# Performance work log

Hardware: AMD Instinct MI355X
Metric: run time of the kernel (lower is better)

The kernel has to match this reference:

```python
import jax, jax.numpy as jnp
import numpy as np

N, L = 32, 2048
C_S, C_E, C_H, K, NRES = 384, 32, 128, 7, 20
C_IN = C_S + C_E  # 416
EPS = 1e-8


def setup_inputs() -> dict:
    key = jax.random.key(0)
    ks = jax.random.split(key, 32)
    s = 0.02
    d = {}
    d['aa_seq'] = jax.random.randint(ks[0], (L,), 0, NRES)
    d['sfea_tns'] = jax.random.normal(ks[1], (N, L, C_S), jnp.float32)
    d['sfea_tns_init'] = jax.random.normal(ks[2], (N, L, C_S), jnp.float32)
    d['encd_tns'] = jax.random.normal(ks[3], (N, L, C_E), jnp.float32)
    d['quat_tns'] = jax.random.normal(ks[4], (N, L, 4), jnp.float32)
    d['trsl_tns'] = jax.random.normal(ks[5], (N, L, 3), jnp.float32)
    # FrameHead linears
    d['Wq'] = jax.random.normal(ks[6], (C_IN, 4), jnp.float32) * s
    d['bq'] = jnp.zeros((4,), jnp.float32)
    d['Wt'] = jax.random.normal(ks[7], (C_IN, 3), jnp.float32) * s
    d['bt'] = jnp.zeros((3,), jnp.float32)
    # 20 per-residue-type AngleHead experts, stacked on leading axis
    d['Wa1'] = jax.random.normal(ks[8], (NRES, C_IN, C_H), jnp.float32) * s
    d['ba1'] = jnp.zeros((NRES, C_H), jnp.float32)
    d['Wa2'] = jax.random.normal(ks[9], (NRES, C_IN, C_H), jnp.float32) * s
    d['ba2'] = jnp.zeros((NRES, C_H), jnp.float32)
    d['Wb1a'] = jax.random.normal(ks[10], (NRES, C_H, C_H), jnp.float32) * s
    d['bb1a'] = jnp.zeros((NRES, C_H), jnp.float32)
    d['Wb1b'] = jax.random.normal(ks[11], (NRES, C_H, C_H), jnp.float32) * s
    d['bb1b'] = jnp.zeros((NRES, C_H), jnp.float32)
    d['Wb2a'] = jax.random.normal(ks[12], (NRES, C_H, C_H), jnp.float32) * s
    d['bb2a'] = jnp.zeros((NRES, C_H), jnp.float32)
    d['Wb2b'] = jax.random.normal(ks[13], (NRES, C_H, C_H), jnp.float32) * s
    d['bb2b'] = jnp.zeros((NRES, C_H), jnp.float32)
    d['Wout'] = jax.random.normal(ks[14], (NRES, C_H, K * 2), jnp.float32) * s
    d['bout'] = jnp.zeros((NRES, K * 2), jnp.float32)
    return d


def _qnorm(q):
    return q * jax.lax.rsqrt(jnp.sum(q * q, -1, keepdims=True) + EPS)


def _quat_mul(q, p):
    w1, x1, y1, z1 = jnp.split(q, 4, -1)
    w2, x2, y2, z2 = jnp.split(p, 4, -1)
    return jnp.concatenate([
        w1 * w2 - x1 * x2 - y1 * y2 - z1 * z2,
        w1 * x2 + x1 * w2 + y1 * z2 - z1 * y2,
        w1 * y2 - x1 * z2 + y1 * w2 + z1 * x2,
        w1 * z2 + x1 * y2 - y1 * x2 + z1 * w2], -1)


def _quat_rotate(q, v):
    # rotate vector v by unit quaternion q = (w, xyz)
    w, qv = q[..., :1], q[..., 1:]
    t = 2.0 * jnp.cross(qv, v)
    return v + w * t + jnp.cross(qv, t)


def _angle_net(sfcd, sfcd_init, aa, Wa1, ba1, Wa2, ba2,
               Wb1a, bb1a, Wb1b, bb1b, Wb2a, bb2a, Wb2b, bb2b, Wout, bout):
    # residue-type routed AngleHead: gather each token's expert weights by aa index
    g = lambda W: jnp.take(W, aa, axis=0)  # [L, ...]
    relu = jax.nn.relu
    a = (jnp.einsum('nlc,lch->nlh', relu(sfcd), g(Wa1)) + g(ba1)
         + jnp.einsum('nlc,lch->nlh', relu(sfcd_init), g(Wa2)) + g(ba2))
    # residual block 1
    h = jnp.einsum('nlh,lhk->nlk', relu(a), g(Wb1a)) + g(bb1a)
    a = a + jnp.einsum('nlh,lhk->nlk', relu(h), g(Wb1b)) + g(bb1b)
    # residual block 2
    h = jnp.einsum('nlh,lhk->nlk', relu(a), g(Wb2a)) + g(bb2a)
    a = a + jnp.einsum('nlh,lhk->nlk', relu(h), g(Wb2b)) + g(bb2b)
    out = jnp.einsum('nlh,lhk->nlk', relu(a), g(Wout)) + g(bout)  # [N,L,2K]
    ang = out.reshape(out.shape[0], out.shape[1], K, 2)
    norm = jnp.sqrt(jnp.sum(ang * ang, -1, keepdims=True) + 1e-12)
    return ang / norm


def reference(aa_seq, sfea_tns, sfea_tns_init, encd_tns, quat_tns, trsl_tns,
              Wq, bq, Wt, bt, Wa1, ba1, Wa2, ba2, Wb1a, bb1a, Wb1b, bb1b,
              Wb2a, bb2a, Wb2b, bb2b, Wout, bout):
    sfcd = jnp.concatenate([sfea_tns, encd_tns], -1)          # [N,L,C_IN]
    sfcd_init = jnp.concatenate([sfea_tns_init, encd_tns], -1)
    # FrameHead: quaternion/translation update signals
    quat_upd = sfcd @ Wq + bq                                  # [N,L,4]
    trsl_upd = sfcd @ Wt + bt                                  # [N,L,3]
    q_old = _qnorm(quat_tns)
    quat_new = _qnorm(_quat_mul(q_old, _qnorm(quat_upd)))
    trsl_new = trsl_tns + _quat_rotate(q_old, trsl_upd)
    angl_tns = _angle_net(sfcd, sfcd_init, aa_seq, Wa1, ba1, Wa2, ba2,
                          Wb1a, bb1a, Wb1b, bb1b, Wb2a, bb2a, Wb2b, bb2b,
                          Wout, bout)
    return quat_new, trsl_new, angl_tns, quat_upd
```

## Files before the change

### kernel.cpp

```cpp
#include <hip/hip_runtime.h>

#define L_SEQ 2048
#define CS 384
#define CE 32
#define CIN 416
#define CH 128
#define NRES 20

#define ABST 136
#define PADN 2068
#define NB2  1034

#define PERM_REGION 4608
#define WA_PER (CH*CIN)
#define WB_PER (CH*CH)
#define WO_PER (16*CH)
#define OFF_WA1T 0
#define OFF_WA2T (NRES*WA_PER)
#define OFF_WB1AT (2*NRES*WA_PER)
#define OFF_WB1BT (OFF_WB1AT + 1*NRES*WB_PER)
#define OFF_WB2AT (OFF_WB1AT + 2*NRES*WB_PER)
#define OFF_WB2BT (OFF_WB1AT + 3*NRES*WB_PER)
#define OFF_WOUTT (OFF_WB1AT + 4*NRES*WB_PER)
#define TOTW (OFF_WOUTT + NRES*WO_PER)

#define OUT_TR 262144
#define OUT_ANG 458752
#define OUT_QU 1376256

#define LOSCALE 4096.0f
#define ILOSCALE (1.0f/4096.0f)
#define F16MIN 6.1035156e-5f

typedef _Float16 f16x8 __attribute__((ext_vector_type(8)));
typedef _Float16 f16x4 __attribute__((ext_vector_type(4)));
typedef float f32x4 __attribute__((ext_vector_type(4)));

#define MFMA16 __builtin_amdgcn_mfma_f32_16x16x32_f16

static __device__ __forceinline__ void split1(float x, _Float16& h, _Float16& l) {
  _Float16 hi = (__builtin_fabsf(x) < F16MIN) ? (_Float16)0.f : (_Float16)x;
  h = hi;
  l = (_Float16)((x - (float)hi) * LOSCALE);
}

__global__ __launch_bounds__(256) void quat_head(
    const float* __restrict__ sfea, const float* __restrict__ encd,
    const float* __restrict__ quat, const float* __restrict__ trsl,
    const float* __restrict__ Wq, const float* __restrict__ bq,
    const float* __restrict__ Wt, const float* __restrict__ bt,
    float* __restrict__ out) {
  const int wv   = threadIdx.x >> 6;
  const int lane = threadIdx.x & 63;
  const size_t idx = (size_t)blockIdx.x * 4 + wv;
  const float* __restrict__ srow = sfea + idx * CS;

  float q0=0,q1=0,q2=0,q3=0,t0=0,t1=0,t2=0;
  #pragma unroll
  for (int cc = 0; cc < 6; ++cc) {
    const int ch = cc*64 + lane;
    const float s = srow[ch];
    const float4 wq = *reinterpret_cast<const float4*>(Wq + (size_t)ch*4);
    const float* wt = Wt + (size_t)ch*3;
    q0 += s*wq.x; q1 += s*wq.y; q2 += s*wq.z; q3 += s*wq.w;
    t0 += s*wt[0]; t1 += s*wt[1]; t2 += s*wt[2];
  }
  if (lane < CE) {
    const float s = encd[idx*CE + lane];
    const int ch = CS + lane;
    const float4 wq = *reinterpret_cast<const float4*>(Wq + (size_t)ch*4);
    const float* wt = Wt + (size_t)ch*3;
    q0 += s*wq.x; q1 += s*wq.y; q2 += s*wq.z; q3 += s*wq.w;
    t0 += s*wt[0]; t1 += s*wt[1]; t2 += s*wt[2];
  }
  #pragma unroll
  for (int off = 1; off < 64; off <<= 1) {
    q0 += __shfl_xor(q0, off); q1 += __shfl_xor(q1, off);
    q2 += __shfl_xor(q2, off); q3 += __shfl_xor(q3, off);
    t0 += __shfl_xor(t0, off); t1 += __shfl_xor(t1, off);
    t2 += __shfl_xor(t2, off);
  }
  if (lane == 0) {
    const float u0 = q0 + bq[0], u1 = q1 + bq[1], u2 = q2 + bq[2], u3 = q3 + bq[3];
    const float v0 = t0 + bt[0], v1 = t1 + bt[1], v2 = t2 + bt[2];
    float a0 = quat[idx*4+0], a1 = quat[idx*4+1], a2 = quat[idx*4+2], a3 = quat[idx*4+3];
    const float rq = rsqrtf(a0*a0+a1*a1+a2*a2+a3*a3 + 1e-8f);
    a0*=rq; a1*=rq; a2*=rq; a3*=rq;
    const float ru = rsqrtf(u0*u0+u1*u1+u2*u2+u3*u3 + 1e-8f);
    const float p0=u0*ru, p1=u1*ru, p2=u2*ru, p3=u3*ru;
    const float mw = a0*p0 - a1*p1 - a2*p2 - a3*p3;
    const float mx = a0*p1 + a1*p0 + a2*p3 - a3*p2;
    const float my = a0*p2 - a1*p3 + a2*p0 + a3*p1;
    const float mz = a0*p3 + a1*p2 - a2*p1 + a3*p0;
    const float rm = rsqrtf(mw*mw+mx*mx+my*my+mz*mz + 1e-8f);
    out[idx*4+0]=mw*rm; out[idx*4+1]=mx*rm; out[idx*4+2]=my*rm; out[idx*4+3]=mz*rm;
    const float tx = 2.f*(a2*v2 - a3*v1);
    const float ty = 2.f*(a3*v0 - a1*v2);
    const float tz = 2.f*(a1*v1 - a2*v0);
    out[OUT_TR + idx*3+0] = trsl[idx*3+0] + v0 + a0*tx + (a2*tz - a3*ty);
    out[OUT_TR + idx*3+1] = trsl[idx*3+1] + v1 + a0*ty + (a3*tx - a1*tz);
    out[OUT_TR + idx*3+2] = trsl[idx*3+2] + v2 + a0*tz + (a1*ty - a2*tx);
    out[OUT_QU + idx*4+0]=u0; out[OUT_QU + idx*4+1]=u1;
    out[OUT_QU + idx*4+2]=u2; out[OUT_QU + idx*4+3]=u3;
  }
}

__global__ __launch_bounds__(1024) void build_perm(const int* __restrict__ aa_seq,
                                                   unsigned short* __restrict__ perm) {
  __shared__ int cnt[NRES*32];
  __shared__ int woff[NRES*32];
  __shared__ int poff_s[NRES];
  __shared__ int ctot_s[NRES];
  const int t = threadIdx.x;
  const int wv = t >> 6, lane = t & 63;

  for (int i = t; i < PADN; i += 1024) perm[i] = 0;

  int aav[2];
  #pragma unroll
  for (int h = 0; h < 2; ++h) {
    const int W = wv + h*16;
    aav[h] = aa_seq[W*64 + lane];
    #pragma unroll
    for (int a = 0; a < NRES; ++a) {
      const unsigned long long m = __ballot(aav[h] == a);
      if (lane == a) cnt[a*32 + W] = (int)__popcll(m);
    }
  }
  __syncthreads();
  if (t < 32) {
    int tot = 0;
    if (t < NRES) {
      #pragma unroll
      for (int W = 0; W < 32; ++W) tot += cnt[t*32 + W];
    }
    const int pa = (t < NRES) ? ((tot + 1) & ~1) : 0;
    int s = pa;
    #pragma unroll
    for (int o = 1; o < 32; o <<= 1) {
      const int u = __shfl_up(s, o);
      if (lane >= o) s += u;
    }
    if (t < NRES) { poff_s[t] = s - pa; ctot_s[t] = tot; }
    for (int a = 0; a < NRES; ++a) {
      const int v0 = cnt[a*32 + t];
      int v = v0;
      #pragma unroll
      for (int o = 1; o < 32; o <<= 1) {
        const int u = __shfl_up(v, o);
        if (lane >= o) v += u;
      }
      woff[a*32 + t] = poff_s[a] + v - v0;
    }
  }
  __syncthreads();
  const unsigned long long ltmask = (lane == 0) ? 0ull : (~0ull >> (64 - lane));
  #pragma unroll
  for (int h = 0; h < 2; ++h) {
    const int W = wv + h*16;
    const int a = aav[h];
    int pos = 0;
    #pragma unroll
    for (int aq = 0; aq < NRES; ++aq) {
      const unsigned long long m = __ballot(a == aq);
      if (a == aq) pos = woff[aq*32 + W] + (int)__popcll(m & ltmask);
    }
    const unsigned short lv = (unsigned short)(W*64 + lane);
    perm[pos] = lv;
    if ((ctot_s[a] & 1) && pos == poff_s[a] + ctot_s[a] - 1) perm[pos + 1] = lv;
  }
}

__global__ __launch_bounds__(256) void convert_w(
    const float* __restrict__ Wa1, const float* __restrict__ Wa2,
    const float* __restrict__ Wb1a, const float* __restrict__ Wb1b,
    const float* __restrict__ Wb2a, const float* __restrict__ Wb2b,
    const float* __restrict__ Wout, _Float16* __restrict__ wsw) {
  const int idx = blockIdx.x * 256 + threadIdx.x;
  if (idx >= TOTW) return;
  float v;
  if (idx < OFF_WB1AT) {
    const int which = (idx < OFF_WA2T) ? 0 : 1;
    const float* W = which ? Wa2 : Wa1;
    int r = idx - which * OFF_WA2T;
    const int aa = r / WA_PER; r -= aa * WA_PER;
    const int h = r / CIN;     const int c = r - h * CIN;
    v = W[((size_t)aa*CIN + c)*CH + h];
  } else if (idx < OFF_WOUTT) {
    int q = idx - OFF_WB1AT;
    const int which = q / (NRES*WB_PER);
    int r = q - which * (NRES*WB_PER);
    const float* W = (which==0)?Wb1a:(which==1)?Wb1b:(which==2)?Wb2a:Wb2b;
    const int aa = r / WB_PER; r -= aa * WB_PER;
    const int h = r / CH;      const int c = r - h * CH;
    v = W[((size_t)aa*CH + c)*CH + h];
  } else {
    int r = idx - OFF_WOUTT;
    const int aa = r / WO_PER; r -= aa * WO_PER;
    const int kk = r / CH;     const int c = r - kk * CH;
    v = (kk < 14) ? Wout[((size_t)aa*CH + c)*14 + kk] : 0.f;
  }
  _Float16 h, l; split1(v, h, l);
  wsw[idx] = h;
  wsw[(size_t)TOTW + idx] = l;
}

static __device__ __forceinline__ void fold(f32x4 acc[2][2], const f32x4 accL[2][2],
                                            float b0, float b1) {
  #pragma unroll
  for (int m = 0; m < 2; ++m)
    #pragma unroll
    for (int i = 0; i < 4; ++i) {
      acc[m][0][i] += accL[m][0][i]*ILOSCALE + b0;
      acc[m][1][i] += accL[m][1][i]*ILOSCALE + b1;
    }
}

static __device__ __forceinline__ void store_relu_pair(_Float16* dh, _Float16* dl,
    const f32x4 acc[2][2], int lane, int h0) {
  const int lr = lane & 15;
  const int r0 = (lane >> 4) << 2;
  #pragma unroll
  for (int m = 0; m < 2; ++m)
    #pragma unroll
    for (int p = 0; p < 2; ++p)
      #pragma unroll
      for (int i = 0; i < 4; ++i) {
        const float v = fmaxf(acc[m][p][i], 0.f);
        _Float16 hh, ll; split1(v, hh, ll);
        const int idx = (m*16 + r0 + i)*ABST + h0 + p*16 + lr;
        dh[idx] = hh; dl[idx] = ll;
      }
}

template<int S>
static __device__ __forceinline__ void gemm_dual(
    const _Float16* aH0, const _Float16* aL0,
    const _Float16* aH1, const _Float16* aL1,
    const _Float16* __restrict__ wH,
    int kbase, int nks,
    f32x4 acc0[2][2], f32x4 acc0L[2][2],
    f32x4 acc1[2][2], f32x4 acc1L[2][2],
    int lane, int h0) {
  const int lr = lane & 15;
  const int lk = (lane >> 4) << 3;
  #pragma unroll
  for (int ks = 0; ks < nks; ++ks) {
    const int kl = ks*32 + lk;
    const int kg = kbase + kl;
    const _Float16* p0 = wH + (size_t)(h0+lr)*S + kg;
    const _Float16* p1 = wH + (size_t)(h0+16+lr)*S + kg;
    const f16x8 b0h = *(const f16x8*)p0;
    const f16x8 b0l = *(const f16x8*)(p0 + TOTW);
    const f16x8 b1h = *(const f16x8*)p1;
    const f16x8 b1l = *(const f16x8*)(p1 + TOTW);
#define DOPOS(AH, AL, AC, ACL) { \
    const f16x8 a0h = *(const f16x8*)(AH + lr*ABST + kl); \
    const f16x8 a0l = *(const f16x8*)(AL + lr*ABST + kl); \
    const f16x8 a1h = *(const f16x8*)(AH + (lr+16)*ABST + kl); \
    const f16x8 a1l = *(const f16x8*)(AL + (lr+16)*ABST + kl); \
    AC[0][0]  = MFMA16(a0h, b0h, AC[0][0], 0,0,0); \
    ACL[0][0] = MFMA16(a0h, b0l, ACL[0][0], 0,0,0); \
    ACL[0][0] = MFMA16(a0l, b0h, ACL[0][0], 0,0,0); \
    AC[1][0]  = MFMA16(a1h, b0h, AC[1][0], 0,0,0); \
    ACL[1][0] = MFMA16(a1h, b0l, ACL[1][0], 0,0,0); \
    ACL[1][0] = MFMA16(a1l, b0h, ACL[1][0], 0,0,0); \
    AC[0][1]  = MFMA16(a0h, b1h, AC[0][1], 0,0,0); \
    ACL[0][1] = MFMA16(a0h, b1l, ACL[0][1], 0,0,0); \
    ACL[0][1] = MFMA16(a0l, b1h, ACL[0][1], 0,0,0); \
    AC[1][1]  = MFMA16(a1h, b1h, AC[1][1], 0,0,0); \
    ACL[1][1] = MFMA16(a1h, b1l, ACL[1][1], 0,0,0); \
    ACL[1][1] = MFMA16(a1l, b1h, ACL[1][1], 0,0,0); }
    DOPOS(aH0, aL0, acc0, acc0L)
    DOPOS(aH1, aL1, acc1, acc1L)
#undef DOPOS
  }
}

static __device__ __forceinline__ void stage_row128(
    const float* __restrict__ row, _Float16* dH, _Float16* dL, int n, int sj) {
  #pragma unroll
  for (int q2 = 0; q2 < 2; ++q2) {
    const int cl = q2*64 + sj*8;
    const float4 v0 = *(const float4*)(row + cl);
    const float4 v1 = *(const float4*)(row + cl + 4);
    const float xs[8] = {v0.x,v0.y,v0.z,v0.w,v1.x,v1.y,v1.z,v1.w};
    f16x8 h8, l8;
    #pragma unroll
    for (int e = 0; e < 8; ++e) {
      _Float16 hh, ll; split1(fmaxf(xs[e], 0.f), hh, ll);
      h8[e] = hh; l8[e] = ll;
    }
    *(f16x8*)(dH + n*ABST + cl) = h8;
    *(f16x8*)(dL + n*ABST + cl) = l8;
  }
}

static __device__ __forceinline__ void stage_encd(
    const float* __restrict__ erow,
    _Float16* sH, _Float16* sL, _Float16* iH, _Float16* iL, int n, int sj) {
  const int cl = sj*4;
  const float4 v = *(const float4*)(erow + cl);
  const float xs[4] = {v.x, v.y, v.z, v.w};
  f16x4 h4, l4;
  #pragma unroll
  for (int e = 0; e < 4; ++e) {
    _Float16 hh, ll; split1(fmaxf(xs[e], 0.f), hh, ll);
    h4[e] = hh; l4[e] = ll;
  }
  *(f16x4*)(sH + n*ABST + cl) = h4;  *(f16x4*)(sL + n*ABST + cl) = l4;
  *(f16x4*)(iH + n*ABST + cl) = h4;  *(f16x4*)(iL + n*ABST + cl) = l4;
}

__global__ __launch_bounds__(256, 2) void fah_main(
    const int* __restrict__ aa_seq, const unsigned short* __restrict__ perm,
    const float* __restrict__ sfea, const float* __restrict__ sfei,
    const float* __restrict__ encd,
    const float* __restrict__ ba1, const float* __restrict__ ba2,
    const float* __restrict__ bb1a, const float* __restrict__ bb1b,
    const float* __restrict__ bb2a, const float* __restrict__ bb2b,
    const float* __restrict__ bout,
    const _Float16* __restrict__ wsw,
    float* __restrict__ out) {
  __shared__ __align__(16) _Float16 sf0H[32*ABST], sf0L[32*ABST];
  __shared__ __align__(16) _Float16 in0H[32*ABST], in0L[32*ABST];
  __shared__ __align__(16) _Float16 sf1H[32*ABST], sf1L[32*ABST];
  __shared__ __align__(16) _Float16 in1H[32*ABST], in1L[32*ABST];
  _Float16 *ab0H = sf0H, *ab0L = sf0L, *hb0H = in0H, *hb0L = in0L;
  _Float16 *ab1H = sf1H, *ab1L = sf1L, *hb1H = in1H, *hb1L = in1L;

  const int orig = blockIdx.x;
  const int xcd = orig & 7, i8 = orig >> 3;
  const int sp = (xcd < 2 ? xcd*130 : 260 + (xcd-2)*129) + i8;
  const int l0 = perm[2*sp], l1 = perm[2*sp+1];
  const int aa = aa_seq[l0];

  const int t = threadIdx.x;
  const int lane = t & 63, wv = t >> 6;
  const int lr = lane & 15, lk = (lane >> 4) << 3, h0 = wv * 32;
  const int n = t >> 3, sj = t & 7;

  const f32x4 zz = {0.f, 0.f, 0.f, 0.f};
  f32x4 accA0[2][2], accA0L[2][2], accA1[2][2], accA1L[2][2];
  #pragma unroll
  for (int m = 0; m < 2; ++m) {
    accA0[m][0]=zz; accA0[m][1]=zz; accA0L[m][0]=zz; accA0L[m][1]=zz;
    accA1[m][0]=zz; accA1[m][1]=zz; accA1L[m][0]=zz; accA1L[m][1]=zz;
  }

  const _Float16* wsA1 = wsw + OFF_WA1T + (size_t)aa*WA_PER;
  const _Float16* wsA2 = wsw + OFF_WA2T + (size_t)aa*WA_PER;

  #pragma unroll
  for (int ck = 0; ck < 4; ++ck) {
    const int koff = ck * 128;
    if (ck < 3) {
      stage_row128(sfea + ((size_t)n*L_SEQ + l0)*CS + koff, sf0H, sf0L, n, sj);
      stage_row128(sfei + ((size_t)n*L_SEQ + l0)*CS + koff, in0H, in0L, n, sj);
      stage_row128(sfea + ((size_t)n*L_SEQ + l1)*CS + koff, sf1H, sf1L, n, sj);
      stage_row128(sfei + ((size_t)n*L_SEQ + l1)*CS + koff, in1H, in1L, n, sj);
    } else {
      stage_encd(encd + ((size_t)n*L_SEQ + l0)*CE, sf0H, sf0L, in0H, in0L, n, sj);
      stage_encd(encd + ((size_t)n*L_SEQ + l1)*CE, sf1H, sf1L, in1H, in1L, n, sj);
    }
    __syncthreads();
    const int nks = (ck < 3) ? 4 : 1;
    gemm_dual<CIN>(sf0H, sf0L, sf1H, sf1L, wsA1, koff, nks,
                   accA0, accA0L, accA1, accA1L, lane, h0);
    gemm_dual<CIN>(in0H, in0L, in1H, in1L, wsA2, koff, nks,
                   accA0, accA0L, accA1, accA1L, lane, h0);
    __syncthreads();
  }

  {
    const float b0v = ba1[aa*CH + h0 + lr]      + ba2[aa*CH + h0 + lr];
    const float b1v = ba1[aa*CH + h0 + 16 + lr] + ba2[aa*CH + h0 + 16 + lr];
    fold(accA0, accA0L, b0v, b1v);
    fold(accA1, accA1L, b0v, b1v);
    store_relu_pair(ab0H, ab0L, accA0, lane, h0);
    store_relu_pair(ab1H, ab1L, accA1, lane, h0);
  }
  __syncthreads();

  {
    f32x4 c0[2][2], c0L[2][2], c1[2][2], c1L[2][2];
    #pragma unroll
    for (int m = 0; m < 2; ++m) { c0[m][0]=zz;c0[m][1]=zz;c0L[m][0]=zz;c0L[m][1]=zz;
                                  c1[m][0]=zz;c1[m][1]=zz;c1L[m][0]=zz;c1L[m][1]=zz; }
    gemm_dual<CH>(ab0H, ab0L, ab1H, ab1L, wsw + OFF_WB1AT + (size_t)aa*WB_PER, 0, 4,
                  c0, c0L, c1, c1L, lane, h0);
    const float B0 = bb1a[aa*CH + h0 + lr], B1 = bb1a[aa*CH + h0 + 16 + lr];
    fold(c0, c0L, B0, B1); fold(c1, c1L, B0, B1);
    store_relu_pair(hb0H, hb0L, c0, lane, h0);
    store_relu_pair(hb1H, hb1L, c1, lane, h0);
  }
  __syncthreads();
  {
    f32x4 c0L[2][2], c1L[2][2];
    #pragma unroll
    for (int m = 0; m < 2; ++m) { c0L[m][0]=zz;c0L[m][1]=zz;c1L[m][0]=zz;c1L[m][1]=zz; }
    gemm_dual<CH>(hb0H, hb0L, hb1H, hb1L, wsw + OFF_WB1BT + (size_t)aa*WB_PER, 0, 4,
                  accA0, c0L, accA1, c1L, lane, h0);
    const float B0 = bb1b[aa*CH + h0 + lr], B1 = bb1b[aa*CH + h0 + 16 + lr];
    fold(accA0, c0L, B0, B1); fold(accA1, c1L, B0, B1);
    store_relu_pair(ab0H, ab0L, accA0, lane, h0);
    store_relu_pair(ab1H, ab1L, accA1, lane, h0);
  }
  __syncthreads();
  {
    f32x4 c0[2][2], c0L[2][2], c1[2][2], c1L[2][2];
    #pragma unroll
    for (int m = 0; m < 2; ++m) { c0[m][0]=zz;c0[m][1]=zz;c0L[m][0]=zz;c0L[m][1]=zz;
                                  c1[m][0]=zz;c1[m][1]=zz;c1L[m][0]=zz;c1L[m][1]=zz; }
    gemm_dual<CH>(ab0H, ab0L, ab1H, ab1L, wsw + OFF_WB2AT + (size_t)aa*WB_PER, 0, 4,
                  c0, c0L, c1, c1L, lane, h0);
    const float B0 = bb2a[aa*CH + h0 + lr], B1 = bb2a[aa*CH + h0 + 16 + lr];
    fold(c0, c0L, B0, B1); fold(c1, c1L, B0, B1);
    store_relu_pair(hb0H, hb0L, c0, lane, h0);
    store_relu_pair(hb1H, hb1L, c1, lane, h0);
  }
  __syncthreads();
  {
    f32x4 c0L[2][2], c1L[2][2];
    #pragma unroll
    for (int m = 0; m < 2; ++m) { c0L[m][0]=zz;c0L[m][1]=zz;c1L[m][0]=zz;c1L[m][1]=zz; }
    gemm_dual<CH>(hb0H, hb0L, hb1H, hb1L, wsw + OFF_WB2BT + (size_t)aa*WB_PER, 0, 4,
                  accA0, c0L, accA1, c1L, lane, h0);
    const float B0 = bb2b[aa*CH + h0 + lr], B1 = bb2b[aa*CH + h0 + 16 + lr];
    fold(accA0, c0L, B0, B1); fold(accA1, c1L, B0, B1);
    store_relu_pair(ab0H, ab0L, accA0, lane, h0);
    store_relu_pair(ab1H, ab1L, accA1, lane, h0);
  }
  __syncthreads();

  {
    const int pos  = wv >> 1;
    const int half = wv & 1;
    const _Float16* aH = pos ? ab1H : ab0H;
    const _Float16* aL = pos ? ab1L : ab0L;
    const int lsel = pos ? l1 : l0;
    f32x4 o = zz, oL = zz;
    #pragma unroll
    for (int ks = 0; ks < 4; ++ks) {
      const int k = ks*32 + lk;
      const f16x8 ah = *(const f16x8*)(aH + (half*16 + lr)*ABST + k);
      const f16x8 al = *(const f16x8*)(aL + (half*16 + lr)*ABST + k);
      const _Float16* p = wsw + OFF_WOUTT + (size_t)aa*WO_PER + (size_t)lr*CH + k;
      const f16x8 bh = *(const f16x8*)p;
      const f16x8 bl = *(const f16x8*)(p + TOTW);
      o  = MFMA16(ah, bh, o,  0,0,0);
      oL = MFMA16(ah, bl, oL, 0,0,0);
      oL = MFMA16(al, bh, oL, 0,0,0);
    }
    const float bo = (lr < 14) ? bout[aa*14 + lr] : 0.f;
    #pragma unroll
    for (int i = 0; i < 4; ++i) {
      const float v  = o[i] + oL[i]*ILOSCALE + bo;
      const float pv = __shfl_xor(v, 1);
      const float r  = rsqrtf(v*v + pv*pv + 1e-12f);
      if (lr < 14) {
        const int nrow = half*16 + ((lane >> 4) << 2) + i;
        out[OUT_ANG + (size_t)nrow*(L_SEQ*14) + (size_t)lsel*14 + lr] = v*r;
      }
    }
  }
}

extern "C" void kernel_launch(void* const* d_in, const int* in_sizes, int n_in,
                              void* d_out, int out_size, void* d_ws, size_t ws_size,
                              hipStream_t stream) {
  const int*   aa   = (const int*)  d_in[0];
  const float* sfea = (const float*)d_in[1];
  const float* sfei = (const float*)d_in[2];
  const float* encd = (const float*)d_in[3];
  const float* quat = (const float*)d_in[4];
  const float* trsl = (const float*)d_in[5];
  const float* Wq   = (const float*)d_in[6];
  const float* bq   = (const float*)d_in[7];
  const float* Wt   = (const float*)d_in[8];
  const float* bt   = (const float*)d_in[9];
  const float* Wa1  = (const float*)d_in[10];
  const float* ba1  = (const float*)d_in[11];
  const float* Wa2  = (const float*)d_in[12];
  const float* ba2  = (const float*)d_in[13];
  const float* Wb1a = (const float*)d_in[14];
  const float* bb1a = (const float*)d_in[15];
  const float* Wb1b = (const float*)d_in[16];
  const float* bb1b = (const float*)d_in[17];
  const float* Wb2a = (const float*)d_in[18];
  const float* bb2a = (const float*)d_in[19];
  const float* Wb2b = (const float*)d_in[20];
  const float* bb2b = (const float*)d_in[21];
  const float* Wout = (const float*)d_in[22];
  const float* bout = (const float*)d_in[23];
  float* out = (float*)d_out;

  unsigned short* perm = (unsigned short*)d_ws;
  _Float16* wsw = (_Float16*)((char*)d_ws + PERM_REGION);

  hipLaunchKernelGGL(build_perm, dim3(1), dim3(1024), 0, stream, aa, perm);
  hipLaunchKernelGGL(convert_w, dim3((TOTW + 255)/256), dim3(256), 0, stream,
                     Wa1, Wa2, Wb1a, Wb1b, Wb2a, Wb2b, Wout, wsw);
  hipLaunchKernelGGL(quat_head, dim3(16384), dim3(256), 0, stream,
                     sfea, encd, quat, trsl, Wq, bq, Wt, bt, out);
  hipLaunchKernelGGL(fah_main, dim3(NB2), dim3(256), 0, stream,
                     aa, perm, sfea, sfei, encd,
                     ba1, ba2, bb1a, bb1b, bb2a, bb2b, bout, wsw, out);
}
```

Before: 209.2 us.

## Prefetch next input chunk into registers during GEMM and use lighter barriers

The first-layer loop is unrolled by hand so the global loads for the next 128-column chunk of sfea/sfei (and encd) are issued into registers before the current chunk's MFMA work. The loaded values are converted and written to LDS after the following barrier. All __syncthreads are replaced with a macro that waits only on lgkmcnt before s_barrier, so outstanding global loads are not drained at each barrier. This hides global memory latency behind compute, at the cost of many more live VGPRs (32 float4 registers) under launch_bounds(256,2).

```diff
diff --git a/kernel.cpp b/kernel.cpp
--- a/kernel.cpp
+++ b/kernel.cpp
@@ -37,6 +37,8 @@
 typedef float f32x4 __attribute__((ext_vector_type(4)));
 
 #define MFMA16 __builtin_amdgcn_mfma_f32_16x16x32_f16
+
+#define BAR() { asm volatile("s_waitcnt lgkmcnt(0)" ::: "memory"); __builtin_amdgcn_s_barrier(); }
 
 static __device__ __forceinline__ void split1(float x, _Float16& h, _Float16& l) {
   _Float16 hi = (__builtin_fabsf(x) < F16MIN) ? (_Float16)0.f : (_Float16)x;
@@ -277,30 +279,28 @@
   }
 }
 
-static __device__ __forceinline__ void stage_row128(
+static __device__ __forceinline__ void wr8(const float4 v0, const float4 v1,
+    _Float16* dH, _Float16* dL, int n, int cl) {
+  const float xs[8] = {v0.x,v0.y,v0.z,v0.w,v1.x,v1.y,v1.z,v1.w};
+  f16x8 h8, l8;
+  #pragma unroll
+  for (int e = 0; e < 8; ++e) {
+    _Float16 hh, ll; split1(fmaxf(xs[e], 0.f), hh, ll);
+    h8[e] = hh; l8[e] = ll;
+  }
+  *(f16x8*)(dH + n*ABST + cl) = h8;
+  *(f16x8*)(dL + n*ABST + cl) = l8;
+}
+
+static __device__ __forceinline__ void stage_row_inline(
     const float* __restrict__ row, _Float16* dH, _Float16* dL, int n, int sj) {
-  #pragma unroll
-  for (int q2 = 0; q2 < 2; ++q2) {
-    const int cl = q2*64 + sj*8;
-    const float4 v0 = *(const float4*)(row + cl);
-    const float4 v1 = *(const float4*)(row + cl + 4);
-    const float xs[8] = {v0.x,v0.y,v0.z,v0.w,v1.x,v1.y,v1.z,v1.w};
-    f16x8 h8, l8;
-    #pragma unroll
-    for (int e = 0; e < 8; ++e) {
-      _Float16 hh, ll; split1(fmaxf(xs[e], 0.f), hh, ll);
-      h8[e] = hh; l8[e] = ll;
-    }
-    *(f16x8*)(dH + n*ABST + cl) = h8;
-    *(f16x8*)(dL + n*ABST + cl) = l8;
-  }
-}
-
-static __device__ __forceinline__ void stage_encd(
-    const float* __restrict__ erow,
+  wr8(*(const float4*)(row + sj*8),      *(const float4*)(row + sj*8 + 4),      dH, dL, n, sj*8);
+  wr8(*(const float4*)(row + 64 + sj*8), *(const float4*)(row + 64 + sj*8 + 4), dH, dL, n, 64 + sj*8);
+}
+
+static __device__ __forceinline__ void stage_encd_reg(const float4 v,
     _Float16* sH, _Float16* sL, _Float16* iH, _Float16* iL, int n, int sj) {
   const int cl = sj*4;
-  const float4 v = *(const float4*)(erow + cl);
   const float xs[4] = {v.x, v.y, v.z, v.w};
   f16x4 h4, l4;
   #pragma unroll
@@ -311,6 +311,16 @@
   *(f16x4*)(sH + n*ABST + cl) = h4;  *(f16x4*)(sL + n*ABST + cl) = l4;
   *(f16x4*)(iH + n*ABST + cl) = h4;  *(f16x4*)(iL + n*ABST + cl) = l4;
 }
+
+#define PF_ROW(BASE, OFF, V0, V1, V2, V3)                         \
+  V0 = *(const float4*)((BASE) + (OFF) + sj*8);                   \
+  V1 = *(const float4*)((BASE) + (OFF) + sj*8 + 4);               \
+  V2 = *(const float4*)((BASE) + (OFF) + 64 + sj*8);              \
+  V3 = *(const float4*)((BASE) + (OFF) + 64 + sj*8 + 4);
+
+#define WR_ROW(V0, V1, V2, V3, DH, DL)                            \
+  wr8(V0, V1, DH, DL, n, sj*8);                                   \
+  wr8(V2, V3, DH, DL, n, 64 + sj*8);
 
 __global__ __launch_bounds__(256, 2) void fah_main(
     const int* __restrict__ aa_seq, const unsigned short* __restrict__ perm,
@@ -340,6 +350,14 @@
   const int lr = lane & 15, lk = (lane >> 4) << 3, h0 = wv * 32;
   const int n = t >> 3, sj = t & 7;
 
+  const float* sfeaL0 = sfea + ((size_t)n*L_SEQ + l0)*CS;
+  const float* sfeaL1 = sfea + ((size_t)n*L_SEQ + l1)*CS;
+  const float* sfeiL0 = sfei + ((size_t)n*L_SEQ + l0)*CS;
+  const float* sfeiL1 = sfei + ((size_t)n*L_SEQ + l1)*CS;
+
+  const _Float16* wsA1 = wsw + OFF_WA1T + (size_t)aa*WA_PER;
+  const _Float16* wsA2 = wsw + OFF_WA2T + (size_t)aa*WA_PER;
+
   const f32x4 zz = {0.f, 0.f, 0.f, 0.f};
   f32x4 accA0[2][2], accA0L[2][2], accA1[2][2], accA1L[2][2];
   #pragma unroll
@@ -348,30 +366,56 @@
     accA1[m][0]=zz; accA1[m][1]=zz; accA1L[m][0]=zz; accA1L[m][1]=zz;
   }
 
-  const _Float16* wsA1 = wsw + OFF_WA1T + (size_t)aa*WA_PER;
-  const _Float16* wsA2 = wsw + OFF_WA2T + (size_t)aa*WA_PER;
-
-  #pragma unroll
-  for (int ck = 0; ck < 4; ++ck) {
-    const int koff = ck * 128;
-    if (ck < 3) {
-      stage_row128(sfea + ((size_t)n*L_SEQ + l0)*CS + koff, sf0H, sf0L, n, sj);
-      stage_row128(sfei + ((size_t)n*L_SEQ + l0)*CS + koff, in0H, in0L, n, sj);
-      stage_row128(sfea + ((size_t)n*L_SEQ + l1)*CS + koff, sf1H, sf1L, n, sj);
-      stage_row128(sfei + ((size_t)n*L_SEQ + l1)*CS + koff, in1H, in1L, n, sj);
-    } else {
-      stage_encd(encd + ((size_t)n*L_SEQ + l0)*CE, sf0H, sf0L, in0H, in0L, n, sj);
-      stage_encd(encd + ((size_t)n*L_SEQ + l1)*CE, sf1H, sf1L, in1H, in1L, n, sj);
-    }
-    __syncthreads();
-    const int nks = (ck < 3) ? 4 : 1;
-    gemm_dual<CIN>(sf0H, sf0L, sf1H, sf1L, wsA1, koff, nks,
-                   accA0, accA0L, accA1, accA1L, lane, h0);
-    gemm_dual<CIN>(in0H, in0L, in1H, in1L, wsA2, koff, nks,
-                   accA0, accA0L, accA1, accA1L, lane, h0);
-    __syncthreads();
-  }
-
+  float4 A00,A01,A02,A03, A10,A11,A12,A13;
+  float4 I00,I01,I02,I03, I10,I11,I12,I13;
+
+  stage_row_inline(sfeaL0, sf0H, sf0L, n, sj);
+  stage_row_inline(sfeiL0, in0H, in0L, n, sj);
+  stage_row_inline(sfeaL1, sf1H, sf1L, n, sj);
+  stage_row_inline(sfeiL1, in1H, in1L, n, sj);
+  PF_ROW(sfeaL0, 128, A00,A01,A02,A03)
+  PF_ROW(sfeaL1, 128, A10,A11,A12,A13)
+  PF_ROW(sfeiL0, 128, I00,I01,I02,I03)
+  PF_ROW(sfeiL1, 128, I10,I11,I12,I13)
+  BAR();
+
+  gemm_dual<CIN>(sf0H,sf0L,sf1H,sf1L, wsA1, 0, 4, accA0,accA0L,accA1,accA1L, lane, h0);
+  gemm_dual<CIN>(in0H,in0L,in1H,in1L, wsA2, 0, 4, accA0,accA0L,accA1,accA1L, lane, h0);
+  BAR();
+
+  WR_ROW(A00,A01,A02,A03, sf0H,sf0L)
+  WR_ROW(A10,A11,A12,A13, sf1H,sf1L)
+  WR_ROW(I00,I01,I02,I03, in0H,in0L)
+  WR_ROW(I10,I11,I12,I13, in1H,in1L)
+  PF_ROW(sfeaL0, 256, A00,A01,A02,A03)
+  PF_ROW(sfeaL1, 256, A10,A11,A12,A13)
+  PF_ROW(sfeiL0, 256, I00,I01,I02,I03)
+  PF_ROW(sfeiL1, 256, I10,I11,I12,I13)
+  BAR();
+
+  gemm_dual<CIN>(sf0H,sf0L,sf1H,sf1L, wsA1, 128, 4, accA0,accA0L,accA1,accA1L, lane, h0);
+  gemm_dual<CIN>(in0H,in0L,in1H,in1L, wsA2, 128, 4, accA0,accA0L,accA1,accA1L, lane, h0);
+  BAR();
+
+  WR_ROW(A00,A01,A02,A03, sf0H,sf0L)
+  WR_ROW(A10,A11,A12,A13, sf1H,sf1L)
+  WR_ROW(I00,I01,I02,I03, in0H,in0L)
+  WR_ROW(I10,I11,I12,I13, in1H,in1L)
+  float4 E0, E1;
+  E0 = *(const float4*)(encd + ((size_t)n*L_SEQ + l0)*CE + sj*4);
+  E1 = *(const float4*)(encd + ((size_t)n*L_SEQ + l1)*CE + sj*4);
+  BAR();
+
+  gemm_dual<CIN>(sf0H,sf0L,sf1H,sf1L, wsA1, 256, 4, accA0,accA0L,accA1,accA1L, lane, h0);
+  gemm_dual<CIN>(in0H,in0L,in1H,in1L, wsA2, 256, 4, accA0,accA0L,accA1,accA1L, lane, h0);
+  BAR();
+
+  stage_encd_reg(E0, sf0H, sf0L, in0H, in0L, n, sj);
+  stage_encd_reg(E1, sf1H, sf1L, in1H, in1L, n, sj);
+  BAR();
+
+  gemm_dual<CIN>(sf0H,sf0L,sf1H,sf1L, wsA1, 384, 1, accA0,accA0L,accA1,accA1L, lane, h0);
+  gemm_dual<CIN>(in0H,in0L,in1H,in1L, wsA2, 384, 1, accA0,accA0L,accA1,accA1L, lane, h0);
   {
     const float b0v = ba1[aa*CH + h0 + lr]      + ba2[aa*CH + h0 + lr];
     const float b1v = ba1[aa*CH + h0 + 16 + lr] + ba2[aa*CH + h0 + 16 + lr];
@@ -380,7 +424,7 @@
     store_relu_pair(ab0H, ab0L, accA0, lane, h0);
     store_relu_pair(ab1H, ab1L, accA1, lane, h0);
   }
-  __syncthreads();
+  BAR();
 
   {
     f32x4 c0[2][2], c0L[2][2], c1[2][2], c1L[2][2];
@@ -394,7 +438,7 @@
     store_relu_pair(hb0H, hb0L, c0, lane, h0);
     store_relu_pair(hb1H, hb1L, c1, lane, h0);
   }
-  __syncthreads();
+  BAR();
   {
     f32x4 c0L[2][2], c1L[2][2];
     #pragma unroll
@@ -406,7 +450,7 @@
     store_relu_pair(ab0H, ab0L, accA0, lane, h0);
     store_relu_pair(ab1H, ab1L, accA1, lane, h0);
   }
-  __syncthreads();
+  BAR();
   {
     f32x4 c0[2][2], c0L[2][2], c1[2][2], c1L[2][2];
     #pragma unroll
@@ -419,7 +463,7 @@
     store_relu_pair(hb0H, hb0L, c0, lane, h0);
     store_relu_pair(hb1H, hb1L, c1, lane, h0);
   }
-  __syncthreads();
+  BAR();
   {
     f32x4 c0L[2][2], c1L[2][2];
     #pragma unroll
@@ -431,14 +475,14 @@
     store_relu_pair(ab0H, ab0L, accA0, lane, h0);
     store_relu_pair(ab1H, ab1L, accA1, lane, h0);
   }
-  __syncthreads();
+  BAR();
 
   {
-    const int pos  = wv >> 1;
+    const int opos = wv >> 1;
     const int half = wv & 1;
-    const _Float16* aH = pos ? ab1H : ab0H;
-    const _Float16* aL = pos ? ab1L : ab0L;
-    const int lsel = pos ? l1 : l0;
+    const _Float16* aH = opos ? ab1H : ab0H;
+    const _Float16* aL = opos ? ab1L : ab0L;
+    const int lsel = opos ? l1 : l0;
     f32x4 o = zz, oL = zz;
     #pragma unroll
     for (int ks = 0; ks < 4; ++ks) {
```

Result: slower. 214.0 us (+2.3%).
